# Kernel optimization log

Measured on AMD Instinct MI355X. Metric: run time of the kernel, lower is better.

## Reference

```python
import jax, jax.numpy as jnp
import numpy as np
from jax import lax

B, C, H, W = 8, 128, 128, 128
KW = 9                      # conv window width (w == h == 9)
PW = (KW - 1) // 2


def _make_kernel(key):
    # torch kaiming_normal_(fan_out) on weight (C,1,KW,C): fan_out = C * KW * C
    std = float(np.sqrt(2.0 / (C * KW * C)))
    # stored directly in WIO layout: [KW, C_in, C_out]
    return (jax.random.normal(key, (KW, C, C), dtype=jnp.float32) * std)


def setup_inputs() -> dict:
    key = jax.random.key(0)
    kx, k1, k2, k3, k4 = jax.random.split(key, 5)
    x = jax.random.normal(kx, (B, C, H, W), dtype=jnp.float32)
    return {
        "x": x,
        "k_td": _make_kernel(k1),
        "k_dt": _make_kernel(k2),
        "k_lr": _make_kernel(k3),
        "k_rl": _make_kernel(k4),
    }


def _row_conv(y, K):
    # y: [B, W, C] -> 1D conv along W, full channel mixing, no bias
    return lax.conv_general_dilated(
        y, K, window_strides=(1,), padding=[(PW, PW)],
        dimension_numbers=("NWC", "WIO", "NWC"))


def _dir_scan(x, K, reverse):
    # x: [B, H, W, C]; sequential recurrence along axis 1:
    #   row[i] = row[i] + relu(conv(row[i-1]))   (row[i-1] already updated)
    if reverse:
        x = x[:, ::-1]
    def step(prev, cur):
        new = cur + jax.nn.relu(_row_conv(prev, K))
        return new, new
    first = x[:, 0]
    _, rest = lax.scan(step, first, jnp.moveaxis(x[:, 1:], 1, 0))
    out = jnp.concatenate([first[:, None], jnp.moveaxis(rest, 0, 1)], axis=1)
    if reverse:
        out = out[:, ::-1]
    return out


def reference(x, k_td, k_dt, k_lr, k_rl):
    y = jnp.transpose(x, (0, 2, 3, 1))        # [B, H, W, C]
    y = _dir_scan(y, k_td, reverse=False)      # top -> down
    y = _dir_scan(y, k_dt, reverse=True)       # down -> top
    yt = jnp.swapaxes(y, 1, 2)                 # [B, W, H, C]
    yt = _dir_scan(yt, k_lr, reverse=False)    # left -> right
    yt = _dir_scan(yt, k_rl, reverse=True)     # right -> left
    y = jnp.swapaxes(yt, 1, 2)
    return jnp.transpose(y, (0, 3, 1, 2))      # back to [B, C, H, W]
```

## Files before the change

### kernel.cpp

```cpp
#include <hip/hip_runtime.h>

#define B_   8
#define C_   128
#define HW_  128
#define KW_  9
#define BLKS 8
#define POSB 16
#define ROWS 24
#define STRD 136
#define BUFE (ROWS * STRD)
#define THREADS 512

typedef __bf16 bf16x8 __attribute__((ext_vector_type(8)));
typedef float  floatx4 __attribute__((ext_vector_type(4)));
typedef unsigned long long u64;

__device__ __forceinline__ unsigned short bf16rn(float f) {
  union { float f; unsigned u; } x; x.f = f;
  return (unsigned short)((x.u + 0x7fffu + ((x.u >> 16) & 1u)) >> 16);
}

__global__ __launch_bounds__(256) void nchw_to_nhwc(const float* __restrict__ x,
                                                    float* __restrict__ y) {
  __shared__ float tile[32][33];
  const int blk = blockIdx.x;
  const int b = blk >> 7, h = blk & 127;
  const int tx = threadIdx.x & 31, ty = threadIdx.x >> 5;
  for (int t = 0; t < 16; ++t) {
    const int c0 = (t >> 2) * 32, w0 = (t & 3) * 32;
#pragma unroll
    for (int i = 0; i < 4; ++i) {
      const int c = c0 + ty + i * 8;
      tile[ty + i * 8][tx] = x[(((long)b * C_ + c) * HW_ + h) * HW_ + w0 + tx];
    }
    __syncthreads();
#pragma unroll
    for (int i = 0; i < 4; ++i) {
      const int w = w0 + ty + i * 8;
      y[(((long)b * HW_ + h) * HW_ + w) * C_ + c0 + tx] = tile[tx][ty + i * 8];
    }
    __syncthreads();
  }
}

__global__ __launch_bounds__(256) void nhwc_to_nchw(const float* __restrict__ y,
                                                    float* __restrict__ out) {
  __shared__ float tile[32][33];
  const int blk = blockIdx.x;
  const int b = blk >> 7, h = blk & 127;
  const int tx = threadIdx.x & 31, ty = threadIdx.x >> 5;
  for (int t = 0; t < 16; ++t) {
    const int w0 = (t >> 2) * 32, c0 = (t & 3) * 32;
#pragma unroll
    for (int i = 0; i < 4; ++i) {
      const int w = w0 + ty + i * 8;
      tile[ty + i * 8][tx] = y[(((long)b * HW_ + h) * HW_ + w) * C_ + c0 + tx];
    }
    __syncthreads();
#pragma unroll
    for (int i = 0; i < 4; ++i) {
      const int c = c0 + ty + i * 8;
      out[(((long)b * C_ + c) * HW_ + h) * HW_ + w0 + tx] = tile[tx][ty + i * 8];
    }
    __syncthreads();
  }
}

__global__ __launch_bounds__(THREADS, 2) void scnn_scan_dir(
    const float* __restrict__ Kg, float* __restrict__ y,
    int* flags, u64* mb,
    const int posStride, const int sStride, const int s0, const int ds,
    const int dirIdx) {
  __shared__ unsigned short prow[2][BUFE];
  __shared__ unsigned short halL[4 * 128];
  __shared__ unsigned short halR[4 * 128];
  __shared__ unsigned short z16[8];
  __shared__ float scratch[4 * 2 * 64 * 4];
  const int tid = threadIdx.x;
  const int bid = blockIdx.x;
  const int batch = bid & 7;
  const int blk = bid >> 3;
  const int p0 = blk * POSB;
  const int lane = tid & 63;
  const int wave = tid >> 6;
  const int kh = wave >> 2;
  const int co2 = wave & 3;
  const int l15 = lane & 15;
  const int quad = lane >> 4;
  const int ybase = batch * (HW_ * HW_ * C_);
  int* flagB = flags + (dirIdx * 8 + batch) * BLKS;

  for (int i = tid; i < 2 * BUFE / 4; i += THREADS)
    ((u64*)prow)[i] = 0ull;
  for (int i = tid; i < (4 * 128 * 2 + 8) / 4; i += THREADS)
    ((u64*)halL)[i] = 0ull;
  for (int i = tid; i < 4 * 128 / 4; i += THREADS) ((u64*)halR)[i] = 0ull;
  if (tid < 2) ((u64*)z16)[tid] = 0ull;

  bf16x8 wfrag[2][KW_][2];
#pragma unroll
  for (int ct = 0; ct < 2; ++ct) {
    const int co0 = co2 * 16 + ct * 64;
#pragma unroll
    for (int kw = 0; kw < KW_; ++kw)
#pragma unroll
      for (int c2 = 0; c2 < 2; ++c2) {
        const int c4 = kh * 2 + c2;
        union { bf16x8 v; unsigned short u[8]; } t;
#pragma unroll
        for (int j = 0; j < 8; ++j)
          t.u[j] = bf16rn(Kg[(kw * 128 + c4 * 32 + quad * 8 + j) * 128 + co0 + l15]);
        wfrag[ct][kw][c2] = t.v;
      }
  }
  __syncthreads();

  for (int i = tid; i < ROWS * 32; i += THREADS) {
    const int row = i >> 5, cg = i & 31;
    const int pos = p0 - 4 + row;
    if (pos >= 0 && pos < HW_) {
      const floatx4 v =
          *(const floatx4*)&y[ybase + s0 * sStride + pos * posStride + cg * 4];
      union { u64 u; unsigned short s[4]; } t;
      t.s[0] = bf16rn(v[0]); t.s[1] = bf16rn(v[1]);
      t.s[2] = bf16rn(v[2]); t.s[3] = bf16rn(v[3]);
      if (row < 4)
        *(u64*)&halL[row * 128 + cg * 4] = t.u;
      else if (row >= 20)
        *(u64*)&halR[(row - 20) * 128 + cg * 4] = t.u;
      else
        *(u64*)&prow[0][row * STRD + cg * 4] = t.u;
    }
  }
  __syncthreads();

  int pb = 0;
#pragma unroll 1
  for (int s = 1; s < HW_; ++s) {
    const int srow = s0 + s * ds;
    const int rowb = ybase + srow * sStride;

    __syncthreads();
    if (tid == 0)
      __hip_atomic_store(&flagB[blk], s - 1, __ATOMIC_RELAXED,
                         __HIP_MEMORY_SCOPE_AGENT);

    floatx4 cur[2];
    if (kh == 0) {
#pragma unroll
      for (int ct = 0; ct < 2; ++ct)
        cur[ct] = *(const floatx4*)&y[rowb + (p0 + l15) * posStride +
                                      co2 * 16 + ct * 64 + quad * 4];
    }

    floatx4 acc[2];
    acc[0] = floatx4{0.f, 0.f, 0.f, 0.f};
    acc[1] = floatx4{0.f, 0.f, 0.f, 0.f};
    const unsigned short* pbase = &prow[pb][l15 * STRD + quad * 8];
#pragma unroll
    for (int kw = 0; kw < KW_; ++kw)
#pragma unroll
      for (int c2 = 0; c2 < 2; ++c2) {
        const int c4 = kh * 2 + c2;
        const bf16x8 b0 = *(const bf16x8*)(pbase + kw * STRD + c4 * 32);
        acc[0] = __builtin_amdgcn_mfma_f32_16x16x32_bf16(wfrag[0][kw][c2], b0,
                                                         acc[0], 0, 0, 0);
        acc[1] = __builtin_amdgcn_mfma_f32_16x16x32_bf16(wfrag[1][kw][c2], b0,
                                                         acc[1], 0, 0, 0);
      }

    if (s >= 2) {
      const int par = (s - 1) & 1;
      if (wave == 7 && blk > 0) {
        if (lane == 0)
          while (__hip_atomic_load(&flagB[blk - 1], __ATOMIC_RELAXED,
                                   __HIP_MEMORY_SCOPE_AGENT) < s - 1)
            __builtin_amdgcn_s_sleep(1);
        __atomic_signal_fence(__ATOMIC_SEQ_CST);
        const int base = ((((batch * BLKS + (blk - 1)) * 2 + 1) * 2 + par) * 4) * 32;
        const u64 v0 = __hip_atomic_load(&mb[base + lane], __ATOMIC_RELAXED,
                                         __HIP_MEMORY_SCOPE_AGENT);
        const u64 v1 = __hip_atomic_load(&mb[base + 64 + lane], __ATOMIC_RELAXED,
                                         __HIP_MEMORY_SCOPE_AGENT);
        *(u64*)&halL[(lane >> 5) * 128 + (lane & 31) * 4] = v0;
        *(u64*)&halL[(2 + (lane >> 5)) * 128 + (lane & 31) * 4] = v1;
      }
      if (wave == 6 && blk < BLKS - 1) {
        if (lane == 0)
          while (__hip_atomic_load(&flagB[blk + 1], __ATOMIC_RELAXED,
                                   __HIP_MEMORY_SCOPE_AGENT) < s - 1)
            __builtin_amdgcn_s_sleep(1);
        __atomic_signal_fence(__ATOMIC_SEQ_CST);
        const int base = ((((batch * BLKS + (blk + 1)) * 2 + 0) * 2 + par) * 4) * 32;
        const u64 v0 = __hip_atomic_load(&mb[base + lane], __ATOMIC_RELAXED,
                                         __HIP_MEMORY_SCOPE_AGENT);
        const u64 v1 = __hip_atomic_load(&mb[base + 64 + lane], __ATOMIC_RELAXED,
                                         __HIP_MEMORY_SCOPE_AGENT);
        *(u64*)&halR[(lane >> 5) * 128 + (lane & 31) * 4] = v0;
        *(u64*)&halR[(2 + (lane >> 5)) * 128 + (lane & 31) * 4] = v1;
      }
    }
    __syncthreads();

    if (blk > 0) {
#pragma unroll
      for (int kw = 0; kw < 4; ++kw) {
        const int hr = l15 + kw;
        const bool v = hr <= 3;
#pragma unroll
        for (int c2 = 0; c2 < 2; ++c2) {
          const int c4 = kh * 2 + c2;
          const unsigned short* sp =
              v ? &halL[hr * 128 + c4 * 32 + quad * 8] : z16;
          const bf16x8 b = *(const bf16x8*)sp;
          acc[0] = __builtin_amdgcn_mfma_f32_16x16x32_bf16(wfrag[0][kw][c2], b,
                                                           acc[0], 0, 0, 0);
          acc[1] = __builtin_amdgcn_mfma_f32_16x16x32_bf16(wfrag[1][kw][c2], b,
                                                           acc[1], 0, 0, 0);
        }
      }
    }
    if (blk < BLKS - 1) {
#pragma unroll
      for (int kw = 5; kw < 9; ++kw) {
        const int hr = l15 + kw - 20;
        const bool v = hr >= 0;
#pragma unroll
        for (int c2 = 0; c2 < 2; ++c2) {
          const int c4 = kh * 2 + c2;
          const unsigned short* sp =
              v ? &halR[hr * 128 + c4 * 32 + quad * 8] : z16;
          const bf16x8 b = *(const bf16x8*)sp;
          acc[0] = __builtin_amdgcn_mfma_f32_16x16x32_bf16(wfrag[0][kw][c2], b,
                                                           acc[0], 0, 0, 0);
          acc[1] = __builtin_amdgcn_mfma_f32_16x16x32_bf16(wfrag[1][kw][c2], b,
                                                           acc[1], 0, 0, 0);
        }
      }
    }

    if (kh == 1) {
#pragma unroll
      for (int ct = 0; ct < 2; ++ct)
        *(floatx4*)&scratch[((co2 * 2 + ct) * 64 + lane) * 4] = acc[ct];
    }
    __syncthreads();

    if (kh == 0) {
#pragma unroll
      for (int ct = 0; ct < 2; ++ct) {
        const floatx4 pz =
            *(const floatx4*)&scratch[((co2 * 2 + ct) * 64 + lane) * 4];
        acc[ct] += pz;
      }

      unsigned short* nxt = prow[pb ^ 1];
      const int par_w = s & 1;
#pragma unroll
      for (int ct = 0; ct < 2; ++ct) {
        const int co0 = co2 * 16 + ct * 64;
        const int pl = l15;
        const int co = co0 + quad * 4;
        const floatx4 a = acc[ct];
        const floatx4 c = cur[ct];
        floatx4 o;
        o[0] = c[0] + (a[0] > 0.f ? a[0] : 0.f);
        o[1] = c[1] + (a[1] > 0.f ? a[1] : 0.f);
        o[2] = c[2] + (a[2] > 0.f ? a[2] : 0.f);
        o[3] = c[3] + (a[3] > 0.f ? a[3] : 0.f);
        *(floatx4*)&y[rowb + (p0 + pl) * posStride + co] = o;
        union { u64 u; unsigned short s[4]; } t;
        t.s[0] = bf16rn(o[0]); t.s[1] = bf16rn(o[1]);
        t.s[2] = bf16rn(o[2]); t.s[3] = bf16rn(o[3]);
        *(u64*)&nxt[(pl + 4) * STRD + co] = t.u;
        if (l15 < 4 && blk > 0) {
          const int mbi =
              ((((batch * BLKS + blk) * 2 + 0) * 2 + par_w) * 4 + l15) * 32 +
              (co2 * 4 + ct * 16 + quad);
          __hip_atomic_store(&mb[mbi], t.u, __ATOMIC_RELAXED,
                             __HIP_MEMORY_SCOPE_AGENT);
        }
        if (l15 >= 12 && blk < BLKS - 1) {
          const int mbi =
              ((((batch * BLKS + blk) * 2 + 1) * 2 + par_w) * 4 + (l15 - 12)) * 32 +
              (co2 * 4 + ct * 16 + quad);
          __hip_atomic_store(&mb[mbi], t.u, __ATOMIC_RELAXED,
                             __HIP_MEMORY_SCOPE_AGENT);
        }
      }
    }
    pb ^= 1;
  }
}

extern "C" void kernel_launch(void* const* d_in, const int* in_sizes, int n_in,
                              void* d_out, int out_size, void* d_ws, size_t ws_size,
                              hipStream_t stream) {
  const float* x = (const float*)d_in[0];
  const float* K[4] = {(const float*)d_in[1], (const float*)d_in[2],
                       (const float*)d_in[3], (const float*)d_in[4]};
  float* out = (float*)d_out;

  char* ws = (char*)d_ws;
  float* y = (float*)ws;
  int* flags = (int*)(ws + 67108864);
  u64* mb = (u64*)(ws + 67108864 + 1024);

  hipMemsetAsync(flags, 0, 1024, stream);
  nchw_to_nhwc<<<B_ * HW_, 256, 0, stream>>>(x, y);

  const int PS[4] = {C_, C_, HW_ * C_, HW_ * C_};
  const int SS[4] = {HW_ * C_, HW_ * C_, C_, C_};
  const int S0[4] = {0, HW_ - 1, 0, HW_ - 1};
  const int DS[4] = {1, -1, 1, -1};
  for (int d = 0; d < 4; ++d)
    scnn_scan_dir<<<B_ * BLKS, THREADS, 0, stream>>>(K[d], y, flags, mb, PS[d],
                                                     SS[d], S0[d], DS[d], d);

  nhwc_to_nchw<<<B_ * HW_, 256, 0, stream>>>(y, out);
}
```

Before: 1.940 ms.

## Split epilogue across both kh waves, defer global store, hoist halo mailbox loads

The partial-sum reduction is now symmetric: each kh wave group swaps one output tile through scratch and finishes half the epilogue, so the work no longer sits on only half the waves. The global store of each row result is deferred to the next iteration, where it can overlap the MFMA loop. The neighbour-block mailbox polling and loads move to the top of the iteration so their latency hides behind the main MFMA chain. Halo buffers get a padded stride, and the deferred store needs an extra final store after the loop.

```diff
diff --git a/kernel.cpp b/kernel.cpp
--- a/kernel.cpp
+++ b/kernel.cpp
@@ -8,6 +8,7 @@
 #define POSB 16
 #define ROWS 24
 #define STRD 136
+#define HSTR 136
 #define BUFE (ROWS * STRD)
 #define THREADS 512
 
@@ -72,8 +73,8 @@
     const int posStride, const int sStride, const int s0, const int ds,
     const int dirIdx) {
   __shared__ unsigned short prow[2][BUFE];
-  __shared__ unsigned short halL[4 * 128];
-  __shared__ unsigned short halR[4 * 128];
+  __shared__ unsigned short halL[4 * HSTR];
+  __shared__ unsigned short halR[4 * HSTR];
   __shared__ unsigned short z16[8];
   __shared__ float scratch[4 * 2 * 64 * 4];
   const int tid = threadIdx.x;
@@ -92,9 +93,10 @@
 
   for (int i = tid; i < 2 * BUFE / 4; i += THREADS)
     ((u64*)prow)[i] = 0ull;
-  for (int i = tid; i < (4 * 128 * 2 + 8) / 4; i += THREADS)
+  for (int i = tid; i < 4 * HSTR / 4; i += THREADS) {
     ((u64*)halL)[i] = 0ull;
-  for (int i = tid; i < 4 * 128 / 4; i += THREADS) ((u64*)halR)[i] = 0ull;
+    ((u64*)halR)[i] = 0ull;
+  }
   if (tid < 2) ((u64*)z16)[tid] = 0ull;
 
   bf16x8 wfrag[2][KW_][2];
@@ -125,14 +127,18 @@
       t.s[0] = bf16rn(v[0]); t.s[1] = bf16rn(v[1]);
       t.s[2] = bf16rn(v[2]); t.s[3] = bf16rn(v[3]);
       if (row < 4)
-        *(u64*)&halL[row * 128 + cg * 4] = t.u;
+        *(u64*)&halL[row * HSTR + cg * 4] = t.u;
       else if (row >= 20)
-        *(u64*)&halR[(row - 20) * 128 + cg * 4] = t.u;
+        *(u64*)&halR[(row - 20) * HSTR + cg * 4] = t.u;
       else
         *(u64*)&prow[0][row * STRD + cg * 4] = t.u;
     }
   }
   __syncthreads();
+
+  const int coMine = co2 * 16 + kh * 64 + quad * 4;
+  floatx4 oPrev = floatx4{0.f, 0.f, 0.f, 0.f};
+  int rowbPrev = 0;
 
   int pb = 0;
 #pragma unroll 1
@@ -145,13 +151,40 @@
       __hip_atomic_store(&flagB[blk], s - 1, __ATOMIC_RELAXED,
                          __HIP_MEMORY_SCOPE_AGENT);
 
-    floatx4 cur[2];
-    if (kh == 0) {
-#pragma unroll
-      for (int ct = 0; ct < 2; ++ct)
-        cur[ct] = *(const floatx4*)&y[rowb + (p0 + l15) * posStride +
-                                      co2 * 16 + ct * 64 + quad * 4];
-    }
+    u64 mv0 = 0, mv1 = 0;
+    const int par = (s - 1) & 1;
+    const bool commL = (wave == 7) && (blk > 0) && (s >= 2);
+    const bool commR = (wave == 6) && (blk < BLKS - 1) && (s >= 2);
+    if (commL) {
+      if (lane == 0)
+        while (__hip_atomic_load(&flagB[blk - 1], __ATOMIC_RELAXED,
+                                 __HIP_MEMORY_SCOPE_AGENT) < s - 1)
+          __builtin_amdgcn_s_sleep(1);
+      __atomic_signal_fence(__ATOMIC_SEQ_CST);
+      const int base = ((((batch * BLKS + (blk - 1)) * 2 + 1) * 2 + par) * 4) * 32;
+      mv0 = __hip_atomic_load(&mb[base + lane], __ATOMIC_RELAXED,
+                              __HIP_MEMORY_SCOPE_AGENT);
+      mv1 = __hip_atomic_load(&mb[base + 64 + lane], __ATOMIC_RELAXED,
+                              __HIP_MEMORY_SCOPE_AGENT);
+    }
+    if (commR) {
+      if (lane == 0)
+        while (__hip_atomic_load(&flagB[blk + 1], __ATOMIC_RELAXED,
+                                 __HIP_MEMORY_SCOPE_AGENT) < s - 1)
+          __builtin_amdgcn_s_sleep(1);
+      __atomic_signal_fence(__ATOMIC_SEQ_CST);
+      const int base = ((((batch * BLKS + (blk + 1)) * 2 + 0) * 2 + par) * 4) * 32;
+      mv0 = __hip_atomic_load(&mb[base + lane], __ATOMIC_RELAXED,
+                              __HIP_MEMORY_SCOPE_AGENT);
+      mv1 = __hip_atomic_load(&mb[base + 64 + lane], __ATOMIC_RELAXED,
+                              __HIP_MEMORY_SCOPE_AGENT);
+    }
+
+    if (s >= 2)
+      *(floatx4*)&y[rowbPrev + (p0 + l15) * posStride + coMine] = oPrev;
+
+    const floatx4 cur =
+        *(const floatx4*)&y[rowb + (p0 + l15) * posStride + coMine];
 
     floatx4 acc[2];
     acc[0] = floatx4{0.f, 0.f, 0.f, 0.f};
@@ -169,36 +202,13 @@
                                                          acc[1], 0, 0, 0);
       }
 
-    if (s >= 2) {
-      const int par = (s - 1) & 1;
-      if (wave == 7 && blk > 0) {
-        if (lane == 0)
-          while (__hip_atomic_load(&flagB[blk - 1], __ATOMIC_RELAXED,
-                                   __HIP_MEMORY_SCOPE_AGENT) < s - 1)
-            __builtin_amdgcn_s_sleep(1);
-        __atomic_signal_fence(__ATOMIC_SEQ_CST);
-        const int base = ((((batch * BLKS + (blk - 1)) * 2 + 1) * 2 + par) * 4) * 32;
-        const u64 v0 = __hip_atomic_load(&mb[base + lane], __ATOMIC_RELAXED,
-                                         __HIP_MEMORY_SCOPE_AGENT);
-        const u64 v1 = __hip_atomic_load(&mb[base + 64 + lane], __ATOMIC_RELAXED,
-                                         __HIP_MEMORY_SCOPE_AGENT);
-        *(u64*)&halL[(lane >> 5) * 128 + (lane & 31) * 4] = v0;
-        *(u64*)&halL[(2 + (lane >> 5)) * 128 + (lane & 31) * 4] = v1;
-      }
-      if (wave == 6 && blk < BLKS - 1) {
-        if (lane == 0)
-          while (__hip_atomic_load(&flagB[blk + 1], __ATOMIC_RELAXED,
-                                   __HIP_MEMORY_SCOPE_AGENT) < s - 1)
-            __builtin_amdgcn_s_sleep(1);
-        __atomic_signal_fence(__ATOMIC_SEQ_CST);
-        const int base = ((((batch * BLKS + (blk + 1)) * 2 + 0) * 2 + par) * 4) * 32;
-        const u64 v0 = __hip_atomic_load(&mb[base + lane], __ATOMIC_RELAXED,
-                                         __HIP_MEMORY_SCOPE_AGENT);
-        const u64 v1 = __hip_atomic_load(&mb[base + 64 + lane], __ATOMIC_RELAXED,
-                                         __HIP_MEMORY_SCOPE_AGENT);
-        *(u64*)&halR[(lane >> 5) * 128 + (lane & 31) * 4] = v0;
-        *(u64*)&halR[(2 + (lane >> 5)) * 128 + (lane & 31) * 4] = v1;
-      }
+    if (commL) {
+      *(u64*)&halL[(lane >> 5) * HSTR + (lane & 31) * 4] = mv0;
+      *(u64*)&halL[(2 + (lane >> 5)) * HSTR + (lane & 31) * 4] = mv1;
+    }
+    if (commR) {
+      *(u64*)&halR[(lane >> 5) * HSTR + (lane & 31) * 4] = mv0;
+      *(u64*)&halR[(2 + (lane >> 5)) * HSTR + (lane & 31) * 4] = mv1;
     }
     __syncthreads();
 
@@ -211,7 +221,7 @@
         for (int c2 = 0; c2 < 2; ++c2) {
           const int c4 = kh * 2 + c2;
           const unsigned short* sp =
-              v ? &halL[hr * 128 + c4 * 32 + quad * 8] : z16;
+              v ? &halL[hr * HSTR + c4 * 32 + quad * 8] : z16;
           const bf16x8 b = *(const bf16x8*)sp;
           acc[0] = __builtin_amdgcn_mfma_f32_16x16x32_bf16(wfrag[0][kw][c2], b,
                                                            acc[0], 0, 0, 0);
@@ -229,7 +239,7 @@
         for (int c2 = 0; c2 < 2; ++c2) {
           const int c4 = kh * 2 + c2;
           const unsigned short* sp =
-              v ? &halR[hr * 128 + c4 * 32 + quad * 8] : z16;
+              v ? &halR[hr * HSTR + c4 * 32 + quad * 8] : z16;
           const bf16x8 b = *(const bf16x8*)sp;
           acc[0] = __builtin_amdgcn_mfma_f32_16x16x32_bf16(wfrag[0][kw][c2], b,
                                                            acc[0], 0, 0, 0);
@@ -239,58 +249,45 @@
       }
     }
 
-    if (kh == 1) {
-#pragma unroll
-      for (int ct = 0; ct < 2; ++ct)
-        *(floatx4*)&scratch[((co2 * 2 + ct) * 64 + lane) * 4] = acc[ct];
-    }
-    __syncthreads();
-
-    if (kh == 0) {
-#pragma unroll
-      for (int ct = 0; ct < 2; ++ct) {
-        const floatx4 pz =
-            *(const floatx4*)&scratch[((co2 * 2 + ct) * 64 + lane) * 4];
-        acc[ct] += pz;
-      }
+    *(floatx4*)&scratch[((co2 * 2 + (1 - kh)) * 64 + lane) * 4] = acc[1 - kh];
+    __syncthreads();
+
+    {
+      const floatx4 pz =
+          *(const floatx4*)&scratch[((co2 * 2 + kh) * 64 + lane) * 4];
+      const floatx4 a = acc[kh] + pz;
 
       unsigned short* nxt = prow[pb ^ 1];
       const int par_w = s & 1;
-#pragma unroll
-      for (int ct = 0; ct < 2; ++ct) {
-        const int co0 = co2 * 16 + ct * 64;
-        const int pl = l15;
-        const int co = co0 + quad * 4;
-        const floatx4 a = acc[ct];
-        const floatx4 c = cur[ct];
-        floatx4 o;
-        o[0] = c[0] + (a[0] > 0.f ? a[0] : 0.f);
-        o[1] = c[1] + (a[1] > 0.f ? a[1] : 0.f);
-        o[2] = c[2] + (a[2] > 0.f ? a[2] : 0.f);
-        o[3] = c[3] + (a[3] > 0.f ? a[3] : 0.f);
-        *(floatx4*)&y[rowb + (p0 + pl) * posStride + co] = o;
-        union { u64 u; unsigned short s[4]; } t;
-        t.s[0] = bf16rn(o[0]); t.s[1] = bf16rn(o[1]);
-        t.s[2] = bf16rn(o[2]); t.s[3] = bf16rn(o[3]);
-        *(u64*)&nxt[(pl + 4) * STRD + co] = t.u;
-        if (l15 < 4 && blk > 0) {
-          const int mbi =
-              ((((batch * BLKS + blk) * 2 + 0) * 2 + par_w) * 4 + l15) * 32 +
-              (co2 * 4 + ct * 16 + quad);
-          __hip_atomic_store(&mb[mbi], t.u, __ATOMIC_RELAXED,
-                             __HIP_MEMORY_SCOPE_AGENT);
-        }
-        if (l15 >= 12 && blk < BLKS - 1) {
-          const int mbi =
-              ((((batch * BLKS + blk) * 2 + 1) * 2 + par_w) * 4 + (l15 - 12)) * 32 +
-              (co2 * 4 + ct * 16 + quad);
-          __hip_atomic_store(&mb[mbi], t.u, __ATOMIC_RELAXED,
-                             __HIP_MEMORY_SCOPE_AGENT);
-        }
-      }
-    }
+      floatx4 o;
+      o[0] = cur[0] + (a[0] > 0.f ? a[0] : 0.f);
+      o[1] = cur[1] + (a[1] > 0.f ? a[1] : 0.f);
+      o[2] = cur[2] + (a[2] > 0.f ? a[2] : 0.f);
+      o[3] = cur[3] + (a[3] > 0.f ? a[3] : 0.f);
+      union { u64 u; unsigned short s[4]; } t;
+      t.s[0] = bf16rn(o[0]); t.s[1] = bf16rn(o[1]);
+      t.s[2] = bf16rn(o[2]); t.s[3] = bf16rn(o[3]);
+      *(u64*)&nxt[(l15 + 4) * STRD + coMine] = t.u;
+      if (l15 < 4 && blk > 0) {
+        const int mbi =
+            ((((batch * BLKS + blk) * 2 + 0) * 2 + par_w) * 4 + l15) * 32 +
+            (co2 * 4 + kh * 16 + quad);
+        __hip_atomic_store(&mb[mbi], t.u, __ATOMIC_RELAXED,
+                           __HIP_MEMORY_SCOPE_AGENT);
+      }
+      if (l15 >= 12 && blk < BLKS - 1) {
+        const int mbi =
+            ((((batch * BLKS + blk) * 2 + 1) * 2 + par_w) * 4 + (l15 - 12)) * 32 +
+            (co2 * 4 + kh * 16 + quad);
+        __hip_atomic_store(&mb[mbi], t.u, __ATOMIC_RELAXED,
+                           __HIP_MEMORY_SCOPE_AGENT);
+      }
+      oPrev = o;
+    }
+    rowbPrev = rowb;
     pb ^= 1;
   }
+  *(floatx4*)&y[rowbPrev + (p0 + l15) * posStride + coMine] = oPrev;
 }
 
 extern "C" void kernel_launch(void* const* d_in, const int* in_sizes, int n_in,
```

New measurement: 1.974 ms. About the same (+1.8%).
